# Performance work log

Hardware: AMD Instinct MI355X
Metric: run time of the kernel (lower is better)

## Reference

```python
import jax, jax.numpy as jnp
import numpy as np

B, L, CIN, COUT, TEMB, N_MODES = 32, 8192, 64, 64, 256, 64
M = N_MODES // 2 + 1  # retained rfft modes = 33
EPS = 1e-5


def setup_inputs() -> dict:
    key = jax.random.key(0)
    ks = jax.random.split(key, 12)
    std_w = float(np.sqrt(1.0 / (2.0 * CIN)))
    # flax Dense default kernel init = lecun_normal ~ normal(std=1/sqrt(fan_in)); plain normal is fine for a reference
    return {
        "x": jax.random.normal(ks[0], (B, L, CIN), jnp.float32),
        "t_emb": jax.random.normal(ks[1], (B, TEMB), jnp.float32),
        # SpectralFreqTimeConv1D params
        "spec_w_real": jax.random.normal(ks[2], (M, CIN, COUT), jnp.float32) * std_w,
        "spec_w_imag": jax.random.normal(ks[3], (M, CIN, COUT), jnp.float32) * std_w,
        "dense_re": jax.random.normal(ks[4], (TEMB, M), jnp.float32) / np.sqrt(TEMB),
        "dense_im": jax.random.normal(ks[5], (TEMB, M), jnp.float32) / np.sqrt(TEMB),
        # TimeConv1D params
        "conv_kernel": jax.random.normal(ks[6], (CIN, COUT), jnp.float32) / np.sqrt(CIN),
        "conv_bias": jnp.zeros((COUT,), jnp.float32),
        "tc_weights": jax.random.normal(ks[7], (COUT, COUT), jnp.float32) * 0.01,  # nn.initializers.normal() stddev=0.01
        "psi_kernel": jax.random.normal(ks[8], (TEMB, 2 * COUT), jnp.float32) / np.sqrt(TEMB),
        # BatchNorm params
        "bn_scale": jnp.ones((COUT,), jnp.float32),
        "bn_bias": jnp.zeros((COUT,), jnp.float32),
    }


def reference(x, t_emb, spec_w_real, spec_w_imag, dense_re, dense_im,
              conv_kernel, conv_bias, tc_weights, psi_kernel, bn_scale, bn_bias):
    b, L_in, _ = x.shape
    n_freq = L_in // 2 + 1

    # ---- SpectralFreqTimeConv1D ----
    x_ft = jnp.fft.rfft(x, axis=-2, norm="forward")            # (b, n_freq, CIN) complex
    t_c = (t_emb @ dense_re) + 1j * (t_emb @ dense_im)         # (b, M) complex
    W = spec_w_real + 1j * spec_w_imag                          # (M, CIN, COUT) complex
    # diagonal-in-mode modulation: equivalent to the eye-based einsum chain
    out_m = t_c[:, :, None] * jnp.einsum("bmi,mio->bmo", x_ft[:, :M, :], W)  # (b, M, COUT)
    out_ft = jnp.zeros((b, n_freq, COUT), jnp.complex64).at[:, :M, :].set(out_m)
    x_spec = jnp.fft.irfft(out_ft, axis=-2, n=L_in, norm="forward")  # (b, L, COUT)

    # ---- TimeConv1D (residual branch) ----
    h = x @ conv_kernel + conv_bias                             # 1x1 conv: (b, L, COUT)
    psi = t_emb @ psi_kernel                                    # (b, 2*COUT)
    w_t, b_t = jnp.split(psi, 2, axis=-1)
    # einsum('ij,bjk,blk->bli', W, diag(w_t), h) == (h * w_t) @ W^T
    x_res = jnp.einsum("blj,ij->bli", h * w_t[:, None, :], tc_weights) + b_t[:, None, :]

    # ---- combine, batchnorm (training: batch stats), activation ----
    out = x_spec + x_res
    mean = out.mean(axis=(0, 1))
    var = out.var(axis=(0, 1))
    out = (out - mean) * jax.lax.rsqrt(var + EPS) * bn_scale + bn_bias
    return jax.nn.relu(out)
```

## Files before the change

kernel.cpp:

```cpp
#include <hip/hip_runtime.h>
#include <hip/hip_fp16.h>

typedef short short8 __attribute__((ext_vector_type(8)));
typedef float f32x4 __attribute__((ext_vector_type(4)));
typedef unsigned int u32;
typedef u32 u32x4 __attribute__((ext_vector_type(4)));
typedef unsigned short u16;

#define BB 32
#define LL 8192
#define TE 256
#define MM 33
#define INVL (1.0f/8192.0f)

#define TBLM_OFF 0
#define TTD_OFF  262144
#define VTB_OFF  589824
#define DD_OFF   720896
#define DD2_OFF  722944
#define BNP_OFF  731200

#define SRED2_OFF 4227072
#define VF_OFF    4491264

static __device__ __forceinline__ u16 f2b(float f) {
  u32 u = __float_as_uint(f);
  return (u16)((u + 0x7FFFu + ((u >> 16) & 1u)) >> 16);
}
static __device__ __forceinline__ u32 pk2(float lo, float hi) {
  return __builtin_amdgcn_perm(__float_as_uint(hi) + 0x8000u,
                               __float_as_uint(lo) + 0x8000u,
                               0x07060302u);
}
static __device__ __forceinline__ float fsin(float rev) {
  float r; asm("v_sin_f32 %0, %1" : "=v"(r) : "v"(rev)); return r;
}
static __device__ __forceinline__ float fcos(float rev) {
  float r; asm("v_cos_f32 %0, %1" : "=v"(r) : "v"(rev)); return r;
}


__global__ __launch_bounds__(256) void k_tbl(float* __restrict__ ws) {
  u16* tb = (u16*)ws;
  u16* tt = (u16*)ws + TTD_OFF * 2;
  int bid = blockIdx.x, tid = threadIdx.x;
  if (bid < 1024) {
    int t = bid * 256 + tid;
    int l = t >> 5, m = (t & 31) + 1;
    float rev = (float)((m * l) & (LL - 1)) * INVL;
    int js = (m == 32) ? 0 : 32 + m;
    tb[l * 64 + m]  = f2b(fcos(rev));
    tb[l * 64 + js] = f2b(fsin(rev));
  } else if (bid < 2048) {
    int t = (bid - 1024) * 256 + tid;
    int m = (t >> 13) + 1, l = t & (LL - 1);
    float rev = (float)((m * l) & (LL - 1)) * INVL;
    int js = (m == 32) ? 0 : 32 + m;
    tt[m * LL + l]  = f2b(fcos(rev));
    tt[js * LL + l] = f2b(fsin(rev));
  } else {
    int t = (bid - 2048) * 256 + tid;
    int r = t >> 13;
    tt[(64 + r) * LL + (t & (LL - 1))] = (r == 0) ? 0x3F80u : 0u;
  }
}

__global__ __launch_bounds__(576) void k_dft(const float* __restrict__ x,
                                             const float* __restrict__ ws,
                                             float* __restrict__ scr) {
  __shared__ __align__(16) u16 sX[2][64 * 136];
  int tid = threadIdx.x;
  int b = blockIdx.x >> 5, chunk = blockIdx.x & 31;
  int l0 = chunk * 256;
  int w = tid >> 6, lane = tid & 63;
  const u16* tt = (const u16*)ws + TTD_OFF * 2;

  f32x4 acc[4];
#pragma unroll
  for (int ct = 0; ct < 4; ++ct) acc[ct] = (f32x4){0.f, 0.f, 0.f, 0.f};

  int arow = lane & 15;
  int kb = (lane >> 4) * 8;
  bool isg = (w >= 5);
  int gi = w - 5;
  bool stg = (tid < 512);
  int sc = tid & 63, lg = (tid >> 6) & 7;

  float vx[16];
  if (stg) {
#pragma unroll
    for (int i = 0; i < 16; ++i)
      vx[i] = x[(b * LL + l0 + lg * 16 + i) * 64 + sc];
    u32 wv[8];
#pragma unroll
    for (int j = 0; j < 8; ++j) wv[j] = pk2(vx[2 * j], vx[2 * j + 1]);
    u32x4* dst = (u32x4*)&sX[0][sc * 136 + lg * 16];
    dst[0] = (u32x4){wv[0], wv[1], wv[2], wv[3]};
    dst[1] = (u32x4){wv[4], wv[5], wv[6], wv[7]};
  }
  __syncthreads();

  if (stg) {
#pragma unroll
    for (int i = 0; i < 16; ++i)
      vx[i] = x[(b * LL + l0 + 128 + lg * 16 + i) * 64 + sc];
  }

#pragma unroll
  for (int kk = 0; kk < 4; ++kk) {
    short8 a = isg
      ? *reinterpret_cast<const short8*>(&sX[0][(gi * 16 + arow) * 136 + kk * 32 + kb])
      : *reinterpret_cast<const short8*>(tt + (w * 16 + arow) * LL + l0 + kk * 32 + kb);
#pragma unroll
    for (int ct = 0; ct < 4; ++ct) {
      short8 bf = *reinterpret_cast<const short8*>(&sX[0][(ct * 16 + arow) * 136 + kk * 32 + kb]);
      acc[ct] = __builtin_amdgcn_mfma_f32_16x16x32_bf16(a, bf, acc[ct], 0, 0, 0);
    }
  }

  if (stg) {
    u32 wv[8];
#pragma unroll
    for (int j = 0; j < 8; ++j) wv[j] = pk2(vx[2 * j], vx[2 * j + 1]);
    u32x4* dst = (u32x4*)&sX[1][sc * 136 + lg * 16];
    dst[0] = (u32x4){wv[0], wv[1], wv[2], wv[3]};
    dst[1] = (u32x4){wv[4], wv[5], wv[6], wv[7]};
  }
  __syncthreads();

#pragma unroll
  for (int kk = 0; kk < 4; ++kk) {
    short8 a = isg
      ? *reinterpret_cast<const short8*>(&sX[1][(gi * 16 + arow) * 136 + kk * 32 + kb])
      : *reinterpret_cast<const short8*>(tt + (w * 16 + arow) * LL + l0 + 128 + kk * 32 + kb);
#pragma unroll
    for (int ct = 0; ct < 4; ++ct) {
      short8 bf = *reinterpret_cast<const short8*>(&sX[1][(ct * 16 + arow) * 136 + kk * 32 + kb]);
      acc[ct] = __builtin_amdgcn_mfma_f32_16x16x32_bf16(a, bf, acc[ct], 0, 0, 0);
    }
  }

  int rowbase = isg ? (65 + gi * 16) : (w * 16);
  int rowb = (lane >> 4) * 4;
  u16* pp = (u16*)scr + (size_t)(b * 32 + chunk) * 129 * 64;
#pragma unroll
  for (int ct = 0; ct < 4; ++ct) {
    int col = ct * 16 + (lane & 15);
#pragma unroll
    for (int r = 0; r < 4; ++r) {
      int sl = rowbase + rowb + r;
      if (isg || sl < 65)
        pp[sl * 64 + col] = __half_as_ushort(__float2half(acc[ct][r]));
    }
  }
}

__global__ __launch_bounds__(256) void k_red1(float* __restrict__ scr) {
  int b = blockIdx.y;
  int p = blockIdx.x * 256 + threadIdx.x;
  if (p >= 4128) return;
  const u32* pb = (const u32*)scr + (size_t)b * 32 * 4128;
  float a0 = 0.f, a1 = 0.f;
#pragma unroll 8
  for (int ch = 0; ch < 32; ++ch) {
    u32 u = pb[ch * 4128 + p];
    __half2 h2 = *reinterpret_cast<const __half2*>(&u);
    float2 f = __half22float2(h2);
    a0 += f.x; a1 += f.y;
  }
  *reinterpret_cast<float2*>(scr + SRED2_OFF + b * 8256 + 2 * p) =
      make_float2(a0, a1);
}

__global__ __launch_bounds__(256) void k_vb(
    const float* __restrict__ t_emb, const float* __restrict__ dre,
    const float* __restrict__ dim_, const float* __restrict__ pk,
    const float* __restrict__ swr, const float* __restrict__ swi,
    const float* __restrict__ ck, const float* __restrict__ cbias,
    const float* __restrict__ tw, float* __restrict__ scr,
    float* __restrict__ ws) {
  __shared__ float smem[12352];
  int tid = threadIdx.x;

  if (blockIdx.x < 33) {
    int m = blockIdx.x;
    float2* sW = (float2*)smem;
    float2* sX = (float2*)(smem + 8192);
    float* sTcb = smem + 8192 + 4096;

    for (int idx = tid; idx < 8192; idx += 256) smem[idx] = t_emb[idx];
    __syncthreads();
    if (tid < 64) {
      int b = tid & 31;
      const float* dd = (tid < 32) ? dre : dim_;
      float a = 0.f;
#pragma unroll 8
      for (int j = 0; j < TE; ++j) a = fmaf(smem[b * 256 + j], dd[j * MM + m], a);
      sTcb[tid] = a;
    }
    __syncthreads();

    for (int idx = tid; idx < 4096; idx += 256)
      sW[idx] = make_float2(swr[m * 4096 + idx], swi[m * 4096 + idx]);
    for (int idx = tid; idx < 2048; idx += 256) {
      int b = idx >> 6, i = idx & 63;
      const float* sr = scr + SRED2_OFF + b * 8256;
      float xr, xi;
      if (m == 0)      { xr = sr[64 * 64 + i] * INVL;  xi = 0.f; }
      else if (m < 32) { xr = sr[m * 64 + i] * INVL;   xi = -sr[(32 + m) * 64 + i] * INVL; }
      else             { xr = sr[32 * 64 + i] * INVL;  xi = -sr[0 * 64 + i] * INVL; }
      sX[idx] = make_float2(xr, xi);
    }
    __syncthreads();

    int w = tid >> 6, lane = tid & 63;
    for (int p = 0; p < 8; ++p) {
      int b = p * 4 + w;
      float a0 = 0.f, a1 = 0.f, a2 = 0.f, a3 = 0.f;
#pragma unroll 16
      for (int i = 0; i < 64; ++i) {
        float2 wv = sW[i * 64 + lane];
        float2 xv = sX[b * 64 + i];
        a0 = fmaf(xv.x, wv.x, a0);
        a1 = fmaf(xv.y, wv.y, a1);
        a2 = fmaf(xv.x, wv.y, a2);
        a3 = fmaf(xv.y, wv.x, a3);
      }
      float ar = a0 - a1, ai = a2 + a3;
      float tcr = sTcb[b], tci = sTcb[32 + b];
      float cr = tcr * ar - tci * ai;
      float ci = tcr * ai + tci * ar;
      if (m == 0) {
        ws[DD2_OFF + b * 64 + lane] = cr;
      } else {
        float crr = 2.f * cr, cii = -2.f * ci;
        int js = (m == 32) ? 0 : 32 + m;
        u16* vtb = (u16*)ws + VTB_OFF * 2 + (b * 64 + lane) * 128;
        vtb[64 + m] = f2b(crr);
        vtb[64 + js] = f2b(cii);
        float* vf = scr + VF_OFF + b * 8192;
        vf[(64 + m) * 64 + lane] = crr;
        vf[(64 + js) * 64 + lane] = cii;
      }
    }
  } else {
    int b = blockIdx.x - 33;
    float* sCkT = smem;
    float* sPtw = smem + 4096;
    float* sTe  = smem + 8192;
    float* sPsi = smem + 8448;

    sTe[tid] = t_emb[b * 256 + tid];
    __syncthreads();
    if (tid < 128) {
      float a = 0.f;
#pragma unroll 8
      for (int j = 0; j < TE; ++j) a = fmaf(sTe[j], pk[j * 128 + tid], a);
      sPsi[tid] = a;
    }
    __syncthreads();
    for (int idx = tid; idx < 4096; idx += 256) {
      int c = idx >> 6, j = idx & 63;
      sCkT[j * 64 + c] = ck[idx];
      sPtw[idx] = sPsi[j] * tw[idx];
    }
    __syncthreads();

    u16* vtb = (u16*)ws + VTB_OFF * 2 + b * 64 * 128;
    float* vf = scr + VF_OFF + b * 8192;
    int lane = tid & 63, w = tid >> 6;
#pragma unroll 4
    for (int it = 0; it < 16; ++it) {
      int o = it * 4 + w;
      float a = 0.f;
#pragma unroll 16
      for (int j = 0; j < 64; ++j)
        a = fmaf(sCkT[j * 64 + lane], sPtw[o * 64 + j], a);
      vtb[o * 128 + lane] = f2b(a);
      vf[lane * 64 + o] = a;
    }
    if (tid < 64) {
      float a = 0.f;
      for (int j = 0; j < 64; ++j) a = fmaf(cbias[j], sPtw[tid * 64 + j], a);
      ws[DD_OFF + b * 64 + tid] = a + sPsi[64 + tid];
    }
  }
}

__global__ __launch_bounds__(256) void k_bn(const float* __restrict__ scr,
                                            float* __restrict__ ws) {
  __shared__ float sVx[64 * 64];
  __shared__ float sGx[64 * 64];
  __shared__ float sS[64 * 64];
  __shared__ float sSum[64];
  __shared__ float sP[4][2][64];
  int tid = threadIdx.x, b = blockIdx.x;
  const float* sr = scr + SRED2_OFF + b * 8256;
  const float* vf = scr + VF_OFF + b * 8192;

  for (int p = tid; p < 4096; p += 256) {
    sVx[p] = vf[p];
    sGx[p] = sr[65 * 64 + p];
    sS[p]  = sr[p];
  }
  if (tid < 64) sSum[tid] = sr[64 * 64 + tid];
  __syncthreads();

  int o = tid & 63, part = tid >> 6;
  float m1 = 0.f, q1 = 0.f, cross = 0.f, vt2 = 0.f;
  for (int ii = 0; ii < 16; ++ii) {
    int i = part * 16 + ii;
    float vx = sVx[i * 64 + o];
    m1 = fmaf(sSum[i], vx, m1);
    float w0 = 0.f, w1 = 0.f, c0 = 0.f, c1 = 0.f;
#pragma unroll
    for (int j = 0; j < 64; j += 2) {
      float va = sVx[j * 64 + o], vb = sVx[(j + 1) * 64 + o];
      w0 = fmaf(sGx[i * 64 + j], va, w0);
      w1 = fmaf(sGx[i * 64 + j + 1], vb, w1);
      c0 = fmaf(sS[i * 64 + j], va, c0);
      c1 = fmaf(sS[i * 64 + j + 1], vb, c1);
    }
    q1 = fmaf(vx, w0 + w1, q1);
    float vt = vf[(64 + i) * 64 + o];
    vt2 = fmaf(vt, vt, vt2);
    cross = fmaf(vt, c0 + c1, cross);
  }
  sP[part][0][o] = m1;
  sP[part][1][o] = q1 + 2.f * cross + 4096.f * vt2;
  __syncthreads();
  if (tid < 64) {
    float m = sP[0][0][tid] + sP[1][0][tid] + sP[2][0][tid] + sP[3][0][tid];
    float q = sP[0][1][tid] + sP[1][1][tid] + sP[2][1][tid] + sP[3][1][tid];
    float D = ws[DD_OFF + b * 64 + tid] + ws[DD2_OFF + b * 64 + tid];
    ws[BNP_OFF + b * 128 + tid]      = m + 8192.f * D;
    ws[BNP_OFF + b * 128 + 64 + tid] = q + 2.f * D * m + 8192.f * D * D;
  }
}

__global__ __launch_bounds__(256) void k_main(const float* __restrict__ x,
                                              const float* __restrict__ ws,
                                              const float* __restrict__ bns,
                                              const float* __restrict__ bnb,
                                              float* __restrict__ out) {
  __shared__ float sD[64];
  __shared__ float sA[64];
  __shared__ float sB[64];
  __shared__ float sPp[4][64];
  __shared__ float sPq[4][64];
  int tid = threadIdx.x, w = tid >> 6, lane = tid & 63;
  int b = blockIdx.x >> 6, rg = blockIdx.x & 63;
  const u16* wsu = (const u16*)ws;

  int kb = (lane >> 4) * 8;
  const u16* vtb = wsu + VTB_OFF * 2 + b * 64 * 128;
  short8 bf[4][4];
#pragma unroll
  for (int kk = 0; kk < 4; ++kk)
#pragma unroll
    for (int ct = 0; ct < 4; ++ct)
      bf[kk][ct] = *reinterpret_cast<const short8*>(
          vtb + (ct * 16 + (lane & 15)) * 128 + kk * 32 + kb);

  {
    int o = tid & 63, g = tid >> 6;
    float pm = 0.f, pq = 0.f;
#pragma unroll
    for (int r = 0; r < 8; ++r) {
      int bb = g * 8 + r;
      pm += ws[BNP_OFF + bb * 128 + o];
      pq += ws[BNP_OFF + bb * 128 + 64 + o];
    }
    sPp[g][o] = pm;
    sPq[g][o] = pq;
  }
  if (tid < 64) sD[tid] = ws[DD_OFF + b * 64 + tid] + ws[DD2_OFF + b * 64 + tid];
  __syncthreads();
  if (tid < 64) {
    const float inv_n = 1.f / (32.f * 8192.f);
    float mean = (sPp[0][tid] + sPp[1][tid] + sPp[2][tid] + sPp[3][tid]) * inv_n;
    float ex2  = (sPq[0][tid] + sPq[1][tid] + sPq[2][tid] + sPq[3][tid]) * inv_n;
    float var = ex2 - mean * mean;
    float istd = rsqrtf(var + 1e-5f);
    float al = istd * bns[tid];
    sA[tid] = al;
    sB[tid] = bnb[tid] - mean * al;
  }
  __syncthreads();

  const u16* tb = wsu;
  int rowb = (lane >> 4) * 4;
  int lbase = rg * 128 + w * 32;

#pragma unroll
  for (int rt = 0; rt < 2; ++rt) {
    int l = lbase + rt * 16 + (lane & 15);
    const float* xq = x + (b * LL + l) * 64;
    float4 u0 = *reinterpret_cast<const float4*>(xq + kb);
    float4 u1 = *reinterpret_cast<const float4*>(xq + kb + 4);
    float4 u2 = *reinterpret_cast<const float4*>(xq + 32 + kb);
    float4 u3 = *reinterpret_cast<const float4*>(xq + 32 + kb + 4);
    union { short8 s; u32 wv[4]; } A0, A1;
    A0.wv[0] = pk2(u0.x, u0.y); A0.wv[1] = pk2(u0.z, u0.w);
    A0.wv[2] = pk2(u1.x, u1.y); A0.wv[3] = pk2(u1.z, u1.w);
    A1.wv[0] = pk2(u2.x, u2.y); A1.wv[1] = pk2(u2.z, u2.w);
    A1.wv[2] = pk2(u3.x, u3.y); A1.wv[3] = pk2(u3.z, u3.w);
    short8 a2 = *reinterpret_cast<const short8*>(tb + l * 64 + kb);
    short8 a3 = *reinterpret_cast<const short8*>(tb + l * 64 + 32 + kb);

    f32x4 acc[4];
#pragma unroll
    for (int ct = 0; ct < 4; ++ct) acc[ct] = (f32x4){0.f, 0.f, 0.f, 0.f};
#pragma unroll
    for (int ct = 0; ct < 4; ++ct) {
      acc[ct] = __builtin_amdgcn_mfma_f32_16x16x32_bf16(A0.s, bf[0][ct], acc[ct], 0, 0, 0);
      acc[ct] = __builtin_amdgcn_mfma_f32_16x16x32_bf16(A1.s, bf[1][ct], acc[ct], 0, 0, 0);
      acc[ct] = __builtin_amdgcn_mfma_f32_16x16x32_bf16(a2, bf[2][ct], acc[ct], 0, 0, 0);
      acc[ct] = __builtin_amdgcn_mfma_f32_16x16x32_bf16(a3, bf[3][ct], acc[ct], 0, 0, 0);
    }
#pragma unroll
    for (int ct = 0; ct < 4; ++ct) {
      int o = ct * 16 + (lane & 15);
      float dd = sD[o], al = sA[o], be = sB[o];
#pragma unroll
      for (int r = 0; r < 4; ++r) {
        float v = acc[ct][r] + dd;
        out[(b * LL + lbase + rt * 16 + rowb + r) * 64 + o] =
            fmaxf(fmaf(v, al, be), 0.f);
      }
    }
  }
}

extern "C" void kernel_launch(void* const* d_in, const int* in_sizes, int n_in,
                              void* d_out, int out_size, void* d_ws, size_t ws_size,
                              hipStream_t stream) {
  const float* x     = (const float*)d_in[0];
  const float* t_emb = (const float*)d_in[1];
  const float* swr   = (const float*)d_in[2];
  const float* swi   = (const float*)d_in[3];
  const float* dre   = (const float*)d_in[4];
  const float* dim_  = (const float*)d_in[5];
  const float* ck    = (const float*)d_in[6];
  const float* cbias = (const float*)d_in[7];
  const float* tw    = (const float*)d_in[8];
  const float* pk    = (const float*)d_in[9];
  const float* bns   = (const float*)d_in[10];
  const float* bnb   = (const float*)d_in[11];
  float* ws  = (float*)d_ws;
  float* out = (float*)d_out;

  k_tbl<<<2560, 256, 0, stream>>>(ws);
  k_dft<<<1024, 576, 0, stream>>>(x, ws, out);
  k_red1<<<dim3(17, 32), 256, 0, stream>>>(out);
  k_vb<<<65, 256, 0, stream>>>(t_emb, dre, dim_, pk, swr, swi,
                               ck, cbias, tw, out, ws);
  k_bn<<<32, 256, 0, stream>>>(out, ws);
  k_main<<<2048, 256, 0, stream>>>(x, ws, bns, bnb, out);
}
```

Before: 102.5 us.

## Compute DC row via scalar sums and move table gen into reduction kernel

The DFT kernel drops its fifth MFMA wave, which multiplied x by a ones/zeros padding row to get the DC term. The column sum is now accumulated in registers during staging and written out through shared memory, so the kernel runs 512 threads and no longer needs the padding rows of the twiddle table. Generation of the l-major twiddle table moves from k_tbl into extra blocks of k_red1, so it runs in the reduction kernel after the DFT instead of before it. The intent is less MFMA and table work on the critical path; the DC term is now summed in fp32 instead of through bf16 MFMA, which slightly changes its numerics.

```diff
diff --git a/kernel.cpp b/kernel.cpp
--- a/kernel.cpp
+++ b/kernel.cpp
@@ -41,135 +41,141 @@
 
 
 __global__ __launch_bounds__(256) void k_tbl(float* __restrict__ ws) {
-  u16* tb = (u16*)ws;
   u16* tt = (u16*)ws + TTD_OFF * 2;
+  int t = blockIdx.x * 256 + threadIdx.x;
+  int m = (t >> 13) + 1, l = t & (LL - 1);
+  float rev = (float)((m * l) & (LL - 1)) * INVL;
+  int js = (m == 32) ? 0 : 32 + m;
+  tt[m * LL + l]  = f2b(fcos(rev));
+  tt[js * LL + l] = f2b(fsin(rev));
+}
+
+__global__ __launch_bounds__(512) void k_dft(const float* __restrict__ x,
+                                             const float* __restrict__ ws,
+                                             float* __restrict__ scr) {
+  __shared__ __align__(16) u16 sX[2][64 * 136];
+  __shared__ float sOnes[8 * 64];
+  int tid = threadIdx.x;
+  int b = blockIdx.x >> 5, chunk = blockIdx.x & 31;
+  int l0 = chunk * 256;
+  int w = tid >> 6, lane = tid & 63;
+  const u16* tt = (const u16*)ws + TTD_OFF * 2;
+
+  f32x4 acc[4];
+#pragma unroll
+  for (int ct = 0; ct < 4; ++ct) acc[ct] = (f32x4){0.f, 0.f, 0.f, 0.f};
+
+  int arow = lane & 15;
+  int kb = (lane >> 4) * 8;
+  bool isg = (w >= 4);
+  int gi = w - 4;
+  int sc = tid & 63, lg = tid >> 6;
+
+  float vx[16];
+  float psum = 0.f;
+#pragma unroll
+  for (int i = 0; i < 16; ++i)
+    vx[i] = x[(b * LL + l0 + lg * 16 + i) * 64 + sc];
+  {
+    u32 wv[8];
+#pragma unroll
+    for (int j = 0; j < 8; ++j) {
+      wv[j] = pk2(vx[2 * j], vx[2 * j + 1]);
+      psum += vx[2 * j] + vx[2 * j + 1];
+    }
+    u32x4* dst = (u32x4*)&sX[0][sc * 136 + lg * 16];
+    dst[0] = (u32x4){wv[0], wv[1], wv[2], wv[3]};
+    dst[1] = (u32x4){wv[4], wv[5], wv[6], wv[7]};
+  }
+  __syncthreads();
+
+#pragma unroll
+  for (int i = 0; i < 16; ++i)
+    vx[i] = x[(b * LL + l0 + 128 + lg * 16 + i) * 64 + sc];
+
+#pragma unroll
+  for (int kk = 0; kk < 4; ++kk) {
+    short8 a = isg
+      ? *reinterpret_cast<const short8*>(&sX[0][(gi * 16 + arow) * 136 + kk * 32 + kb])
+      : *reinterpret_cast<const short8*>(tt + (w * 16 + arow) * LL + l0 + kk * 32 + kb);
+#pragma unroll
+    for (int ct = 0; ct < 4; ++ct) {
+      short8 bf = *reinterpret_cast<const short8*>(&sX[0][(ct * 16 + arow) * 136 + kk * 32 + kb]);
+      acc[ct] = __builtin_amdgcn_mfma_f32_16x16x32_bf16(a, bf, acc[ct], 0, 0, 0);
+    }
+  }
+
+  {
+    u32 wv[8];
+#pragma unroll
+    for (int j = 0; j < 8; ++j) {
+      wv[j] = pk2(vx[2 * j], vx[2 * j + 1]);
+      psum += vx[2 * j] + vx[2 * j + 1];
+    }
+    u32x4* dst = (u32x4*)&sX[1][sc * 136 + lg * 16];
+    dst[0] = (u32x4){wv[0], wv[1], wv[2], wv[3]};
+    dst[1] = (u32x4){wv[4], wv[5], wv[6], wv[7]};
+  }
+  sOnes[tid >> 6 == lg ? tid : tid] = psum;
+  __syncthreads();
+
+#pragma unroll
+  for (int kk = 0; kk < 4; ++kk) {
+    short8 a = isg
+      ? *reinterpret_cast<const short8*>(&sX[1][(gi * 16 + arow) * 136 + kk * 32 + kb])
+      : *reinterpret_cast<const short8*>(tt + (w * 16 + arow) * LL + l0 + 128 + kk * 32 + kb);
+#pragma unroll
+    for (int ct = 0; ct < 4; ++ct) {
+      short8 bf = *reinterpret_cast<const short8*>(&sX[1][(ct * 16 + arow) * 136 + kk * 32 + kb]);
+      acc[ct] = __builtin_amdgcn_mfma_f32_16x16x32_bf16(a, bf, acc[ct], 0, 0, 0);
+    }
+  }
+
+  int rowbase = isg ? (65 + gi * 16) : (w * 16);
+  int rowb = (lane >> 4) * 4;
+  u16* pp = (u16*)scr + (size_t)(b * 32 + chunk) * 129 * 64;
+#pragma unroll
+  for (int ct = 0; ct < 4; ++ct) {
+    int col = ct * 16 + (lane & 15);
+#pragma unroll
+    for (int r = 0; r < 4; ++r)
+      pp[(rowbase + rowb + r) * 64 + col] = __half_as_ushort(__float2half(acc[ct][r]));
+  }
+  if (tid < 64) {
+    float s = 0.f;
+#pragma unroll
+    for (int g = 0; g < 8; ++g) s += sOnes[g * 64 + tid];
+    pp[64 * 64 + tid] = __half_as_ushort(__float2half(s));
+  }
+}
+
+__global__ __launch_bounds__(256) void k_red1(float* __restrict__ scr,
+                                              float* __restrict__ ws) {
   int bid = blockIdx.x, tid = threadIdx.x;
-  if (bid < 1024) {
-    int t = bid * 256 + tid;
+  if (bid < 544) {
+    int b = bid / 17, rx = bid % 17;
+    int p = rx * 256 + tid;
+    if (p >= 4128) return;
+    const u32* pb = (const u32*)scr + (size_t)b * 32 * 4128;
+    float a0 = 0.f, a1 = 0.f;
+#pragma unroll 8
+    for (int ch = 0; ch < 32; ++ch) {
+      u32 u = pb[ch * 4128 + p];
+      __half2 h2 = *reinterpret_cast<const __half2*>(&u);
+      float2 f = __half22float2(h2);
+      a0 += f.x; a1 += f.y;
+    }
+    *reinterpret_cast<float2*>(scr + SRED2_OFF + b * 8256 + 2 * p) =
+        make_float2(a0, a1);
+  } else {
+    u16* tb = (u16*)ws;
+    int t = (bid - 544) * 256 + tid;
     int l = t >> 5, m = (t & 31) + 1;
     float rev = (float)((m * l) & (LL - 1)) * INVL;
     int js = (m == 32) ? 0 : 32 + m;
     tb[l * 64 + m]  = f2b(fcos(rev));
     tb[l * 64 + js] = f2b(fsin(rev));
-  } else if (bid < 2048) {
-    int t = (bid - 1024) * 256 + tid;
-    int m = (t >> 13) + 1, l = t & (LL - 1);
-    float rev = (float)((m * l) & (LL - 1)) * INVL;
-    int js = (m == 32) ? 0 : 32 + m;
-    tt[m * LL + l]  = f2b(fcos(rev));
-    tt[js * LL + l] = f2b(fsin(rev));
-  } else {
-    int t = (bid - 2048) * 256 + tid;
-    int r = t >> 13;
-    tt[(64 + r) * LL + (t & (LL - 1))] = (r == 0) ? 0x3F80u : 0u;
-  }
-}
-
-__global__ __launch_bounds__(576) void k_dft(const float* __restrict__ x,
-                                             const float* __restrict__ ws,
-                                             float* __restrict__ scr) {
-  __shared__ __align__(16) u16 sX[2][64 * 136];
-  int tid = threadIdx.x;
-  int b = blockIdx.x >> 5, chunk = blockIdx.x & 31;
-  int l0 = chunk * 256;
-  int w = tid >> 6, lane = tid & 63;
-  const u16* tt = (const u16*)ws + TTD_OFF * 2;
-
-  f32x4 acc[4];
-#pragma unroll
-  for (int ct = 0; ct < 4; ++ct) acc[ct] = (f32x4){0.f, 0.f, 0.f, 0.f};
-
-  int arow = lane & 15;
-  int kb = (lane >> 4) * 8;
-  bool isg = (w >= 5);
-  int gi = w - 5;
-  bool stg = (tid < 512);
-  int sc = tid & 63, lg = (tid >> 6) & 7;
-
-  float vx[16];
-  if (stg) {
-#pragma unroll
-    for (int i = 0; i < 16; ++i)
-      vx[i] = x[(b * LL + l0 + lg * 16 + i) * 64 + sc];
-    u32 wv[8];
-#pragma unroll
-    for (int j = 0; j < 8; ++j) wv[j] = pk2(vx[2 * j], vx[2 * j + 1]);
-    u32x4* dst = (u32x4*)&sX[0][sc * 136 + lg * 16];
-    dst[0] = (u32x4){wv[0], wv[1], wv[2], wv[3]};
-    dst[1] = (u32x4){wv[4], wv[5], wv[6], wv[7]};
-  }
-  __syncthreads();
-
-  if (stg) {
-#pragma unroll
-    for (int i = 0; i < 16; ++i)
-      vx[i] = x[(b * LL + l0 + 128 + lg * 16 + i) * 64 + sc];
-  }
-
-#pragma unroll
-  for (int kk = 0; kk < 4; ++kk) {
-    short8 a = isg
-      ? *reinterpret_cast<const short8*>(&sX[0][(gi * 16 + arow) * 136 + kk * 32 + kb])
-      : *reinterpret_cast<const short8*>(tt + (w * 16 + arow) * LL + l0 + kk * 32 + kb);
-#pragma unroll
-    for (int ct = 0; ct < 4; ++ct) {
-      short8 bf = *reinterpret_cast<const short8*>(&sX[0][(ct * 16 + arow) * 136 + kk * 32 + kb]);
-      acc[ct] = __builtin_amdgcn_mfma_f32_16x16x32_bf16(a, bf, acc[ct], 0, 0, 0);
-    }
-  }
-
-  if (stg) {
-    u32 wv[8];
-#pragma unroll
-    for (int j = 0; j < 8; ++j) wv[j] = pk2(vx[2 * j], vx[2 * j + 1]);
-    u32x4* dst = (u32x4*)&sX[1][sc * 136 + lg * 16];
-    dst[0] = (u32x4){wv[0], wv[1], wv[2], wv[3]};
-    dst[1] = (u32x4){wv[4], wv[5], wv[6], wv[7]};
-  }
-  __syncthreads();
-
-#pragma unroll
-  for (int kk = 0; kk < 4; ++kk) {
-    short8 a = isg
-      ? *reinterpret_cast<const short8*>(&sX[1][(gi * 16 + arow) * 136 + kk * 32 + kb])
-      : *reinterpret_cast<const short8*>(tt + (w * 16 + arow) * LL + l0 + 128 + kk * 32 + kb);
-#pragma unroll
-    for (int ct = 0; ct < 4; ++ct) {
-      short8 bf = *reinterpret_cast<const short8*>(&sX[1][(ct * 16 + arow) * 136 + kk * 32 + kb]);
-      acc[ct] = __builtin_amdgcn_mfma_f32_16x16x32_bf16(a, bf, acc[ct], 0, 0, 0);
-    }
-  }
-
-  int rowbase = isg ? (65 + gi * 16) : (w * 16);
-  int rowb = (lane >> 4) * 4;
-  u16* pp = (u16*)scr + (size_t)(b * 32 + chunk) * 129 * 64;
-#pragma unroll
-  for (int ct = 0; ct < 4; ++ct) {
-    int col = ct * 16 + (lane & 15);
-#pragma unroll
-    for (int r = 0; r < 4; ++r) {
-      int sl = rowbase + rowb + r;
-      if (isg || sl < 65)
-        pp[sl * 64 + col] = __half_as_ushort(__float2half(acc[ct][r]));
-    }
-  }
-}
-
-__global__ __launch_bounds__(256) void k_red1(float* __restrict__ scr) {
-  int b = blockIdx.y;
-  int p = blockIdx.x * 256 + threadIdx.x;
-  if (p >= 4128) return;
-  const u32* pb = (const u32*)scr + (size_t)b * 32 * 4128;
-  float a0 = 0.f, a1 = 0.f;
-#pragma unroll 8
-  for (int ch = 0; ch < 32; ++ch) {
-    u32 u = pb[ch * 4128 + p];
-    __half2 h2 = *reinterpret_cast<const __half2*>(&u);
-    float2 f = __half22float2(h2);
-    a0 += f.x; a1 += f.y;
-  }
-  *reinterpret_cast<float2*>(scr + SRED2_OFF + b * 8256 + 2 * p) =
-      make_float2(a0, a1);
+  }
 }
 
 __global__ __launch_bounds__(256) void k_vb(
@@ -450,9 +456,9 @@
   float* ws  = (float*)d_ws;
   float* out = (float*)d_out;
 
-  k_tbl<<<2560, 256, 0, stream>>>(ws);
-  k_dft<<<1024, 576, 0, stream>>>(x, ws, out);
-  k_red1<<<dim3(17, 32), 256, 0, stream>>>(out);
+  k_tbl<<<1024, 256, 0, stream>>>(ws);
+  k_dft<<<1024, 512, 0, stream>>>(x, ws, out);
+  k_red1<<<1568, 256, 0, stream>>>(out, ws);
   k_vb<<<65, 256, 0, stream>>>(t_emb, dre, dim_, pk, swr, swi,
                                ck, cbias, tw, out, ws);
   k_bn<<<32, 256, 0, stream>>>(out, ws);
```

New measurement: 99.78 us. 1.03x faster.
